# Performance work log

Measured on AMD Instinct MI355X. Metric: run time of the kernel, lower is better.

The kernel has to match this reference:

```python
import jax, jax.numpy as jnp
import numpy as np

N = 65536          # nodes
E = 1048576        # edges
IN_C = 128
HID_C = 32
HEADS = 4
OUT_C = 64
NEG_SLOPE = 0.2
EPS = 1e-16


def gat_conv(x, edge_index, W, att_src, att_dst, bias, heads, out_c, concat):
    """PyG-style GATConv. x: [N, F_in]; edge_index: [2, E] (row=src, col=dst).
    W: [F_in, heads*out_c]; att_src/att_dst: [heads, out_c]; bias: [heads*out_c] or [out_c]."""
    src, dst = edge_index[0], edge_index[1]
    n = x.shape[0]
    h = (x @ W).reshape(n, heads, out_c)                      # [N, H, C]
    a_src = jnp.einsum('nhc,hc->nh', h, att_src)              # [N, H]
    a_dst = jnp.einsum('nhc,hc->nh', h, att_dst)              # [N, H]
    alpha = a_src[src] + a_dst[dst]                           # [E, H]
    alpha = jax.nn.leaky_relu(alpha, NEG_SLOPE)
    # segment softmax over incoming edges of each destination node
    amax = jax.ops.segment_max(alpha, dst, num_segments=n)    # [N, H]
    alpha = jnp.exp(alpha - amax[dst])
    denom = jax.ops.segment_sum(alpha, dst, num_segments=n)   # [N, H]
    alpha = alpha / (denom[dst] + EPS)
    # weighted scatter-add aggregation
    msgs = alpha[:, :, None] * h[src]                         # [E, H, C]
    out = jax.ops.segment_sum(msgs, dst, num_segments=n)      # [N, H, C]
    if concat:
        out = out.reshape(n, heads * out_c)
    else:
        out = out.mean(axis=1)
    return out + bias


def setup_inputs() -> dict:
    key = jax.random.key(0)
    ks = jax.random.split(key, 10)
    s_in = 1.0 / np.sqrt(IN_C)
    s_h = 1.0 / np.sqrt(HEADS * HID_C)
    x = jax.random.normal(ks[0], (N, IN_C), dtype=jnp.float32)
    edge_index = jax.random.randint(ks[1], (2, E), 0, N, dtype=jnp.int64)
    W1 = jax.random.normal(ks[2], (IN_C, HEADS * HID_C), dtype=jnp.float32) * s_in
    att_src1 = jax.random.normal(ks[3], (HEADS, HID_C), dtype=jnp.float32) * s_h
    att_dst1 = jax.random.normal(ks[4], (HEADS, HID_C), dtype=jnp.float32) * s_h
    b1 = jnp.zeros((HEADS * HID_C,), dtype=jnp.float32)
    W2 = jax.random.normal(ks[5], (HEADS * HID_C, OUT_C), dtype=jnp.float32) * s_h
    att_src2 = jax.random.normal(ks[6], (1, OUT_C), dtype=jnp.float32) * s_h
    att_dst2 = jax.random.normal(ks[7], (1, OUT_C), dtype=jnp.float32) * s_h
    b2 = jnp.zeros((OUT_C,), dtype=jnp.float32)
    return {"x": x, "edge_index": edge_index, "W1": W1, "att_src1": att_src1,
            "att_dst1": att_dst1, "b1": b1, "W2": W2, "att_src2": att_src2,
            "att_dst2": att_dst2, "b2": b2}


def reference(x, edge_index, W1, att_src1, att_dst1, b1, W2, att_src2, att_dst2, b2):
    # dropout is identity in eval mode
    h = gat_conv(x, edge_index, W1, att_src1, att_dst1, b1, HEADS, HID_C, concat=True)
    h = jax.nn.sigmoid(h)
    h = gat_conv(h, edge_index, W2, att_src2, att_dst2, b2, 1, OUT_C, concat=True)
    return jax.nn.sigmoid(h)
```

## Files before the change

### kernel.cpp

```cpp
#include <hip/hip_runtime.h>
#include <hip/hip_fp16.h>

#define N_NODES 65536
#define N_EDGES 1048576
#define NBUCK 256
#define PBLOCKS 1024
#define EPB (N_EDGES / PBLOCKS)
#define K4CAP 6144
#define GB1 (N_NODES / 64)
constexpr float NEG = 0.2f;
constexpr float EPS_ = 1e-16f;
constexpr float WSHIFT = 2.7725887f;

typedef __attribute__((ext_vector_type(8))) short bf16x8;
typedef __attribute__((ext_vector_type(4))) float f32x4;

__device__ __forceinline__ unsigned short f2bf(float f) {
    unsigned int u = __float_as_uint(f);
    return (unsigned short)((u + 0x7fffu + ((u >> 16) & 1u)) >> 16);
}
__device__ __forceinline__ unsigned short f2h(float f) {
    __half_raw r = __half_raw(__float2half(f));
    return r.x;
}
__device__ __forceinline__ __half2 u2h2(unsigned int u) {
    union { unsigned int u; __half2 h; } c; c.u = u; return c.h;
}
__device__ __forceinline__ unsigned int h22u(__half2 h) {
    union { unsigned int u; __half2 h; } c; c.h = h; return c.u;
}
__device__ __forceinline__ float lrelu_exp_s(float l) {
    return __expf(fmaxf(l, NEG * l) - WSHIFT);
}


__global__ __launch_bounds__(1024) void scan_a(const int* __restrict__ in,
                                               int* __restrict__ out,
                                               int* __restrict__ bsum) {
    __shared__ int sm[1024];
    int t = threadIdx.x, i = blockIdx.x * 1024 + t;
    int v = in[i];
    sm[t] = v;
    __syncthreads();
    for (int off = 1; off < 1024; off <<= 1) {
        int u = (t >= off) ? sm[t - off] : 0;
        __syncthreads();
        sm[t] += u;
        __syncthreads();
    }
    out[i] = sm[t] - v;
    if (t == 1023) bsum[blockIdx.x] = sm[t];
}

__global__ __launch_bounds__(1024) void scan_c(int* __restrict__ arr,
                                               const int* __restrict__ bsum) {
    __shared__ int partial[4];
    int t = threadIdx.x;
    if (t < 256) {
        int v = (t < (int)blockIdx.x) ? bsum[t] : 0;
        #pragma unroll
        for (int msk = 1; msk < 64; msk <<= 1) v += __shfl_xor(v, msk);
        if ((t & 63) == 0) partial[t >> 6] = v;
    }
    __syncthreads();
    int pref = partial[0] + partial[1] + partial[2] + partial[3];
    arr[blockIdx.x * 1024 + t] += pref;
}

__global__ __launch_bounds__(256) void partition_kernel(const int* __restrict__ ei,
                                                        const int* __restrict__ cursor_mat,
                                                        unsigned int* __restrict__ edge_part) {
    __shared__ int h[NBUCK];
    __shared__ int start[NBUCK];
    __shared__ int cur[NBUCK];
    __shared__ int gcur[NBUCK];
    __shared__ unsigned int stage[EPB];
    int t = threadIdx.x;
    h[t] = 0;
    gcur[t] = cursor_mat[t * PBLOCKS + blockIdx.x];
    __syncthreads();
    unsigned int ent[EPB / 256];
    int base = blockIdx.x * EPB;
    #pragma unroll
    for (int i = 0; i < EPB / 256; ++i) {
        int e = base + i * 256 + t;
        int s = ei[e], d = ei[N_EDGES + e];
        ent[i] = ((unsigned int)s << 16) | (unsigned int)d;
        atomicAdd(&h[d >> 8], 1);
    }
    __syncthreads();
    int v = h[t];
    start[t] = v;
    __syncthreads();
    for (int off = 1; off < 256; off <<= 1) {
        int u = (t >= off) ? start[t - off] : 0;
        __syncthreads();
        start[t] += u;
        __syncthreads();
    }
    int excl = start[t] - v;
    start[t] = excl;
    cur[t] = excl;
    __syncthreads();
    #pragma unroll
    for (int i = 0; i < EPB / 256; ++i) {
        int b = (int)((ent[i] & 0xffffu) >> 8);
        int slot = atomicAdd(&cur[b], 1);
        stage[slot] = ent[i];
    }
    __syncthreads();
    int s0 = t * (EPB / 256);
    #pragma unroll
    for (int i = 0; i < EPB / 256; ++i) {
        unsigned int p = stage[s0 + i];
        int b = (int)((p & 0xffffu) >> 8);
        edge_part[gcur[b] + (s0 + i - start[b])] = p;
    }
}

__global__ __launch_bounds__(1024) void finalize_kernel(const unsigned int* __restrict__ edge_part,
                                                        const int* __restrict__ cursor_mat,
                                                        int* __restrict__ row_ptr,
                                                        unsigned short* __restrict__ csr16) {
    __shared__ int h[256];
    __shared__ int sc[256];
    __shared__ int cur[256];
    __shared__ unsigned short stage[K4CAP];
    int t = threadIdx.x;
    int b = blockIdx.x;
    if (b == NBUCK - 1 && t == 0) row_ptr[N_NODES] = N_EDGES;
    int cs = cursor_mat[b * PBLOCKS];
    int ce = (b == NBUCK - 1) ? N_EDGES : cursor_mat[(b + 1) * PBLOCKS];
    int cnt = ce - cs;
    if (t < 256) h[t] = 0;
    __syncthreads();
    for (int i = t; i < cnt; i += 1024)
        atomicAdd(&h[edge_part[cs + i] & 0xffu], 1);
    __syncthreads();
    int v = 0;
    if (t < 256) { v = h[t]; sc[t] = v; }
    __syncthreads();
    for (int off = 1; off < 256; off <<= 1) {
        int u = (t < 256 && t >= off) ? sc[t - off] : 0;
        __syncthreads();
        if (t < 256) sc[t] += u;
        __syncthreads();
    }
    if (t < 256) {
        int excl = sc[t] - v;
        row_ptr[b * 256 + t] = cs + excl;
        cur[t] = excl;
    }
    __syncthreads();
    if (cnt <= K4CAP) {
        for (int i = t; i < cnt; i += 1024) {
            unsigned int p = edge_part[cs + i];
            int slot = atomicAdd(&cur[p & 0xffu], 1);
            stage[slot] = (unsigned short)(p >> 16);
        }
        __syncthreads();
        for (int i = t; i < cnt; i += 1024)
            csr16[cs + i] = stage[i];
    } else {
        for (int i = t; i < cnt; i += 1024) {
            unsigned int p = edge_part[cs + i];
            int slot = atomicAdd(&cur[p & 0xffu], 1);
            csr16[cs + slot] = (unsigned short)(p >> 16);
        }
    }
}


__global__ __launch_bounds__(256) void gemm1_hist(const float* __restrict__ X,
                                                  const float* __restrict__ W,
                                                  const float* __restrict__ as_w,
                                                  const float* __restrict__ ad_w,
                                                  const int* __restrict__ ei,
                                                  unsigned short* __restrict__ H,
                                                  float* __restrict__ a_src,
                                                  float* __restrict__ a_dst,
                                                  int* __restrict__ hist_mat) {
    extern __shared__ unsigned short Wl[];
    int t = threadIdx.x;
    if (blockIdx.x >= GB1) {
        int* hs = (int*)Wl;
        int pb = blockIdx.x - GB1;
        hs[t] = 0;
        __syncthreads();
        int base = pb * EPB;
        #pragma unroll
        for (int i = 0; i < EPB / 256; ++i) {
            int d = ei[N_EDGES + base + i * 256 + t];
            atomicAdd(&hs[d >> 8], 1);
        }
        __syncthreads();
        hist_mat[t * PBLOCKS + pb] = hs[t];
        return;
    }
    constexpr int OUTC = 128;
    constexpr int NT = OUTC / 16;
    for (int idx = t; idx < OUTC * 128; idx += 256) {
        int j = idx & 7;
        int ln = (idx >> 3) & 63;
        int fc = idx >> 9;
        int kc = fc & 3, ct = fc >> 2;
        int k = kc * 32 + (ln >> 4) * 8 + j;
        int nn = ct * 16 + (ln & 15);
        Wl[idx] = (unsigned short)f2bf(W[k * OUTC + nn]);
    }
    __syncthreads();
    int wave = t >> 6, lane = t & 63;
    int m = lane & 15, quad = lane >> 4;
    int node_base = blockIdx.x * 64 + wave * 16;
    const float* xrow = X + (size_t)(node_base + m) * 128 + quad * 8;
    bf16x8 a[4];
    #pragma unroll
    for (int kc = 0; kc < 4; ++kc) {
        float4 u = *(const float4*)(xrow + kc * 32);
        float4 v = *(const float4*)(xrow + kc * 32 + 4);
        bf16x8 af;
        af[0] = (short)f2bf(u.x); af[1] = (short)f2bf(u.y);
        af[2] = (short)f2bf(u.z); af[3] = (short)f2bf(u.w);
        af[4] = (short)f2bf(v.x); af[5] = (short)f2bf(v.y);
        af[6] = (short)f2bf(v.z); af[7] = (short)f2bf(v.w);
        a[kc] = af;
    }
    float asv[NT], adv[NT];
    #pragma unroll
    for (int ct = 0; ct < NT; ++ct) {
        asv[ct] = as_w[ct * 16 + m];
        adv[ct] = ad_w[ct * 16 + m];
    }
    float ps[4][4] = {};
    float pd[4][4] = {};
    #pragma unroll
    for (int ct = 0; ct < NT; ++ct) {
        f32x4 acc = {0.f, 0.f, 0.f, 0.f};
        #pragma unroll
        for (int kc = 0; kc < 4; ++kc) {
            bf16x8 bfr = *(const bf16x8*)(Wl + ((ct * 4 + kc) * 64 + lane) * 8);
            acc = __builtin_amdgcn_mfma_f32_16x16x32_bf16(a[kc], bfr, acc, 0, 0, 0);
        }
        int hh = ct >> 1;
        #pragma unroll
        for (int r = 0; r < 4; ++r) {
            H[(size_t)(node_base + quad * 4 + r) * OUTC + ct * 16 + m] = f2h(acc[r]);
            ps[r][hh] += acc[r] * asv[ct];
            pd[r][hh] += acc[r] * adv[ct];
        }
    }
    #pragma unroll
    for (int r = 0; r < 4; ++r) {
        #pragma unroll
        for (int hh = 0; hh < 4; ++hh) {
            float s = ps[r][hh], d = pd[r][hh];
            #pragma unroll
            for (int msk = 1; msk < 16; msk <<= 1) {
                s += __shfl_xor(s, msk);
                d += __shfl_xor(d, msk);
            }
            if (m == 0) {
                int node = node_base + quad * 4 + r;
                a_src[node * 4 + hh] = s;
                a_dst[node * 4 + hh] = d;
            }
        }
    }
}


__global__ __launch_bounds__(256) void gemm2_mfma(const unsigned short* __restrict__ X,
                                                  const float* __restrict__ W,
                                                  const float* __restrict__ as_w,
                                                  const float* __restrict__ ad_w,
                                                  unsigned short* __restrict__ H,
                                                  float* __restrict__ a_src,
                                                  float* __restrict__ a_dst) {
    constexpr int OUTC = 64;
    constexpr int NT = OUTC / 16;
    extern __shared__ unsigned short Wl[];
    int t = threadIdx.x;
    for (int idx = t; idx < OUTC * 128; idx += 256) {
        int j = idx & 7;
        int ln = (idx >> 3) & 63;
        int fc = idx >> 9;
        int kc = fc & 3, ct = fc >> 2;
        int k = kc * 32 + (ln >> 4) * 8 + j;
        int nn = ct * 16 + (ln & 15);
        Wl[idx] = (unsigned short)f2bf(W[k * OUTC + nn]);
    }
    __syncthreads();
    int wave = t >> 6, lane = t & 63;
    int m = lane & 15, quad = lane >> 4;
    int node_base = blockIdx.x * 64 + wave * 16;
    const unsigned short* xrow = X + (size_t)(node_base + m) * 128 + quad * 8;
    bf16x8 a[4];
    #pragma unroll
    for (int kc = 0; kc < 4; ++kc) a[kc] = *(const bf16x8*)(xrow + kc * 32);
    float asv[NT], adv[NT];
    #pragma unroll
    for (int ct = 0; ct < NT; ++ct) {
        asv[ct] = as_w[ct * 16 + m];
        adv[ct] = ad_w[ct * 16 + m];
    }
    float ps[4] = {};
    float pd[4] = {};
    #pragma unroll
    for (int ct = 0; ct < NT; ++ct) {
        f32x4 acc = {0.f, 0.f, 0.f, 0.f};
        #pragma unroll
        for (int kc = 0; kc < 4; ++kc) {
            bf16x8 bfr = *(const bf16x8*)(Wl + ((ct * 4 + kc) * 64 + lane) * 8);
            acc = __builtin_amdgcn_mfma_f32_16x16x32_bf16(a[kc], bfr, acc, 0, 0, 0);
        }
        #pragma unroll
        for (int r = 0; r < 4; ++r) {
            H[(size_t)(node_base + quad * 4 + r) * OUTC + ct * 16 + m] = f2h(acc[r]);
            ps[r] += acc[r] * asv[ct];
            pd[r] += acc[r] * adv[ct];
        }
    }
    #pragma unroll
    for (int r = 0; r < 4; ++r) {
        float s = ps[r], d = pd[r];
        #pragma unroll
        for (int msk = 1; msk < 16; msk <<= 1) {
            s += __shfl_xor(s, msk);
            d += __shfl_xor(d, msk);
        }
        if (m == 0) {
            int node = node_base + quad * 4 + r;
            a_src[node] = s;
            a_dst[node] = d;
        }
    }
}


__global__ __launch_bounds__(256, 8) void agg1_kernel(const int* __restrict__ row_ptr,
                                                      const unsigned short* __restrict__ csr16,
                                                      const unsigned int* __restrict__ h1u,
                                                      const float* __restrict__ a_src,
                                                      const float* __restrict__ a_dst,
                                                      const float* __restrict__ b1,
                                                      unsigned short* __restrict__ x2) {
    int wave = (blockIdx.x * 256 + threadIdx.x) >> 6;
    int lane = threadIdx.x & 63;
    int half = lane >> 5;
    int ln = lane & 31;
    int n = wave * 2 + half;
    int j8 = ln & 7;
    int whead = ln >> 3;
    int sub = ln >> 4;
    int col = ln & 15;
    int hd_c = col >> 2;
    int rbase = half * 32 + hd_c * 8 + sub;
    float adw = a_dst[n * 4 + whead];
    const unsigned int* h1c = h1u + col * 4;
    const float* asw = a_src + whead;
    int e = row_ptr[n], end = row_ptr[n + 1];
    __half2 acc0 = u2h2(0u), acc1 = u2h2(0u), acc2 = u2h2(0u), acc3 = u2h2(0u);
    float denom = 0.f;
    while (e < end) {
        int rem = end - e;
        int mbA = rem > 8 ? 8 : rem;
        int remB = rem - 8;
        int mbB = remB > 8 ? 8 : (remB > 0 ? remB : 0);
        int idxA = e + (j8 < mbA ? j8 : 0);
        int idxB = (remB > 0) ? (e + 8 + (j8 < mbB ? j8 : 0)) : idxA;
        int sA = (int)csr16[idxA];
        int sB = (int)csr16[idxB];
        float lA = asw[sA * 4] + adw;
        float lB = asw[sB * 4] + adw;
        float wA = (j8 < mbA) ? lrelu_exp_s(lA) : 0.f;
        float wB = (j8 < mbB) ? lrelu_exp_s(lB) : 0.f;
        denom += wA + wB;
        unsigned int curA = ((unsigned int)f2h(wA) << 16) | (unsigned int)sA;
        unsigned int curB = ((unsigned int)f2h(wB) << 16) | (unsigned int)sB;
        unsigned int pkA0 = __shfl(curA, rbase);
        unsigned int pkA1 = __shfl(curA, rbase + 2);
        unsigned int pkA2 = __shfl(curA, rbase + 4);
        unsigned int pkA3 = __shfl(curA, rbase + 6);
        unsigned int pkB0 = __shfl(curB, rbase);
        unsigned int pkB1 = __shfl(curB, rbase + 2);
        unsigned int pkB2 = __shfl(curB, rbase + 4);
        unsigned int pkB3 = __shfl(curB, rbase + 6);
        uint4 hvA0 = *(const uint4*)(h1c + (size_t)(pkA0 & 0xffffu) * 64);
        uint4 hvA1 = *(const uint4*)(h1c + (size_t)(pkA1 & 0xffffu) * 64);
        uint4 hvA2 = *(const uint4*)(h1c + (size_t)(pkA2 & 0xffffu) * 64);
        uint4 hvA3 = *(const uint4*)(h1c + (size_t)(pkA3 & 0xffffu) * 64);
        uint4 hvB0 = *(const uint4*)(h1c + (size_t)(pkB0 & 0xffffu) * 64);
        uint4 hvB1 = *(const uint4*)(h1c + (size_t)(pkB1 & 0xffffu) * 64);
        uint4 hvB2 = *(const uint4*)(h1c + (size_t)(pkB2 & 0xffffu) * 64);
        uint4 hvB3 = *(const uint4*)(h1c + (size_t)(pkB3 & 0xffffu) * 64);
        unsigned int wu; __half2 w2;
        wu = pkA0 >> 16; w2 = u2h2(wu | (wu << 16));
        acc0 = __hfma2(w2, u2h2(hvA0.x), acc0);
        acc1 = __hfma2(w2, u2h2(hvA0.y), acc1);
        acc2 = __hfma2(w2, u2h2(hvA0.z), acc2);
        acc3 = __hfma2(w2, u2h2(hvA0.w), acc3);
        wu = pkA1 >> 16; w2 = u2h2(wu | (wu << 16));
        acc0 = __hfma2(w2, u2h2(hvA1.x), acc0);
        acc1 = __hfma2(w2, u2h2(hvA1.y), acc1);
        acc2 = __hfma2(w2, u2h2(hvA1.z), acc2);
        acc3 = __hfma2(w2, u2h2(hvA1.w), acc3);
        wu = pkA2 >> 16; w2 = u2h2(wu | (wu << 16));
        acc0 = __hfma2(w2, u2h2(hvA2.x), acc0);
        acc1 = __hfma2(w2, u2h2(hvA2.y), acc1);
        acc2 = __hfma2(w2, u2h2(hvA2.z), acc2);
        acc3 = __hfma2(w2, u2h2(hvA2.w), acc3);
        wu = pkA3 >> 16; w2 = u2h2(wu | (wu << 16));
        acc0 = __hfma2(w2, u2h2(hvA3.x), acc0);
        acc1 = __hfma2(w2, u2h2(hvA3.y), acc1);
        acc2 = __hfma2(w2, u2h2(hvA3.z), acc2);
        acc3 = __hfma2(w2, u2h2(hvA3.w), acc3);
        wu = pkB0 >> 16; w2 = u2h2(wu | (wu << 16));
        acc0 = __hfma2(w2, u2h2(hvB0.x), acc0);
        acc1 = __hfma2(w2, u2h2(hvB0.y), acc1);
        acc2 = __hfma2(w2, u2h2(hvB0.z), acc2);
        acc3 = __hfma2(w2, u2h2(hvB0.w), acc3);
        wu = pkB1 >> 16; w2 = u2h2(wu | (wu << 16));
        acc0 = __hfma2(w2, u2h2(hvB1.x), acc0);
        acc1 = __hfma2(w2, u2h2(hvB1.y), acc1);
        acc2 = __hfma2(w2, u2h2(hvB1.z), acc2);
        acc3 = __hfma2(w2, u2h2(hvB1.w), acc3);
        wu = pkB2 >> 16; w2 = u2h2(wu | (wu << 16));
        acc0 = __hfma2(w2, u2h2(hvB2.x), acc0);
        acc1 = __hfma2(w2, u2h2(hvB2.y), acc1);
        acc2 = __hfma2(w2, u2h2(hvB2.z), acc2);
        acc3 = __hfma2(w2, u2h2(hvB2.w), acc3);
        wu = pkB3 >> 16; w2 = u2h2(wu | (wu << 16));
        acc0 = __hfma2(w2, u2h2(hvB3.x), acc0);
        acc1 = __hfma2(w2, u2h2(hvB3.y), acc1);
        acc2 = __hfma2(w2, u2h2(hvB3.z), acc2);
        acc3 = __hfma2(w2, u2h2(hvB3.w), acc3);
        e += 16;
    }
    acc0 = __hadd2(acc0, u2h2(__shfl_xor(h22u(acc0), 16)));
    acc1 = __hadd2(acc1, u2h2(__shfl_xor(h22u(acc1), 16)));
    acc2 = __hadd2(acc2, u2h2(__shfl_xor(h22u(acc2), 16)));
    acc3 = __hadd2(acc3, u2h2(__shfl_xor(h22u(acc3), 16)));
    #pragma unroll
    for (int m = 1; m < 8; m <<= 1) denom += __shfl_xor(denom, m);
    float dfin = __shfl(denom, half * 32 + hd_c * 8);
    if (sub == 0) {
        float inv = 1.f / (dfin + EPS_);
        int c0 = col * 8;
        float v[8];
        v[0] = __low2float(acc0); v[1] = __high2float(acc0);
        v[2] = __low2float(acc1); v[3] = __high2float(acc1);
        v[4] = __low2float(acc2); v[5] = __high2float(acc2);
        v[6] = __low2float(acc3); v[7] = __high2float(acc3);
        unsigned int o[4];
        #pragma unroll
        for (int i = 0; i < 4; ++i) {
            float u0 = v[2 * i] * inv + b1[c0 + 2 * i];
            float u1 = v[2 * i + 1] * inv + b1[c0 + 2 * i + 1];
            u0 = 1.f / (1.f + __expf(-u0));
            u1 = 1.f / (1.f + __expf(-u1));
            o[i] = (unsigned int)f2bf(u0) | ((unsigned int)f2bf(u1) << 16);
        }
        *(uint4*)(x2 + (size_t)n * 128 + c0) = make_uint4(o[0], o[1], o[2], o[3]);
    }
}

__global__ __launch_bounds__(256, 8) void agg2_kernel(const int* __restrict__ row_ptr,
                                                      const unsigned short* __restrict__ csr16,
                                                      const unsigned int* __restrict__ h2u,
                                                      const float* __restrict__ a_src,
                                                      const float* __restrict__ a_dst,
                                                      const float* __restrict__ b2,
                                                      float* __restrict__ out) {
    int wave = (blockIdx.x * 256 + threadIdx.x) >> 6;
    int lane = threadIdx.x & 63;
    int half = lane >> 5;
    int ln = lane & 31;
    int n = wave * 2 + half;
    int j8 = ln & 7;
    int sub = (ln >> 3) & 3;
    int col = ln & 7;
    int rbase = half * 32 + sub;
    float ad = a_dst[n];
    const unsigned int* h2c = h2u + col * 4;
    int e = row_ptr[n], end = row_ptr[n + 1];
    __half2 acc0 = u2h2(0u), acc1 = u2h2(0u), acc2 = u2h2(0u), acc3 = u2h2(0u);
    float denom = 0.f;
    while (e < end) {
        int rem = end - e;
        int mbA = rem > 8 ? 8 : rem;
        int remB = rem - 8;
        int mbB = remB > 8 ? 8 : (remB > 0 ? remB : 0);
        int idxA = e + (j8 < mbA ? j8 : 0);
        int idxB = (remB > 0) ? (e + 8 + (j8 < mbB ? j8 : 0)) : idxA;
        int sA = (int)csr16[idxA];
        int sB = (int)csr16[idxB];
        float lA = a_src[sA] + ad;
        float lB = a_src[sB] + ad;
        float wA = (j8 < mbA) ? lrelu_exp_s(lA) : 0.f;
        float wB = (j8 < mbB) ? lrelu_exp_s(lB) : 0.f;
        denom += wA + wB;
        unsigned int curA = ((unsigned int)f2h(wA) << 16) | (unsigned int)sA;
        unsigned int curB = ((unsigned int)f2h(wB) << 16) | (unsigned int)sB;
        unsigned int pkA0 = __shfl(curA, rbase);
        unsigned int pkA1 = __shfl(curA, rbase + 4);
        unsigned int pkB0 = __shfl(curB, rbase);
        unsigned int pkB1 = __shfl(curB, rbase + 4);
        uint4 hvA0 = *(const uint4*)(h2c + (size_t)(pkA0 & 0xffffu) * 32);
        uint4 hvA1 = *(const uint4*)(h2c + (size_t)(pkA1 & 0xffffu) * 32);
        uint4 hvB0 = *(const uint4*)(h2c + (size_t)(pkB0 & 0xffffu) * 32);
        uint4 hvB1 = *(const uint4*)(h2c + (size_t)(pkB1 & 0xffffu) * 32);
        unsigned int wu; __half2 w2;
        wu = pkA0 >> 16; w2 = u2h2(wu | (wu << 16));
        acc0 = __hfma2(w2, u2h2(hvA0.x), acc0);
        acc1 = __hfma2(w2, u2h2(hvA0.y), acc1);
        acc2 = __hfma2(w2, u2h2(hvA0.z), acc2);
        acc3 = __hfma2(w2, u2h2(hvA0.w), acc3);
        wu = pkA1 >> 16; w2 = u2h2(wu | (wu << 16));
        acc0 = __hfma2(w2, u2h2(hvA1.x), acc0);
        acc1 = __hfma2(w2, u2h2(hvA1.y), acc1);
        acc2 = __hfma2(w2, u2h2(hvA1.z), acc2);
        acc3 = __hfma2(w2, u2h2(hvA1.w), acc3);
        wu = pkB0 >> 16; w2 = u2h2(wu | (wu << 16));
        acc0 = __hfma2(w2, u2h2(hvB0.x), acc0);
        acc1 = __hfma2(w2, u2h2(hvB0.y), acc1);
        acc2 = __hfma2(w2, u2h2(hvB0.z), acc2);
        acc3 = __hfma2(w2, u2h2(hvB0.w), acc3);
        wu = pkB1 >> 16; w2 = u2h2(wu | (wu << 16));
        acc0 = __hfma2(w2, u2h2(hvB1.x), acc0);
        acc1 = __hfma2(w2, u2h2(hvB1.y), acc1);
        acc2 = __hfma2(w2, u2h2(hvB1.z), acc2);
        acc3 = __hfma2(w2, u2h2(hvB1.w), acc3);
        e += 16;
    }
    #pragma unroll
    for (int m = 8; m < 32; m <<= 1) {
        acc0 = __hadd2(acc0, u2h2(__shfl_xor(h22u(acc0), m)));
        acc1 = __hadd2(acc1, u2h2(__shfl_xor(h22u(acc1), m)));
        acc2 = __hadd2(acc2, u2h2(__shfl_xor(h22u(acc2), m)));
        acc3 = __hadd2(acc3, u2h2(__shfl_xor(h22u(acc3), m)));
    }
    #pragma unroll
    for (int m = 1; m < 8; m <<= 1) denom += __shfl_xor(denom, m);
    if (sub == 0) {
        float inv = 1.f / (denom + EPS_);
        int c0 = col * 8;
        float v[8];
        v[0] = __low2float(acc0); v[1] = __high2float(acc0);
        v[2] = __low2float(acc1); v[3] = __high2float(acc1);
        v[4] = __low2float(acc2); v[5] = __high2float(acc2);
        v[6] = __low2float(acc3); v[7] = __high2float(acc3);
        float o[8];
        #pragma unroll
        for (int i = 0; i < 8; ++i) {
            float u = v[i] * inv + b2[c0 + i];
            o[i] = 1.f / (1.f + __expf(-u));
        }
        float4* dst = (float4*)(out + (size_t)n * 64 + c0);
        dst[0] = make_float4(o[0], o[1], o[2], o[3]);
        dst[1] = make_float4(o[4], o[5], o[6], o[7]);
    }
}


extern "C" void kernel_launch(void* const* d_in, const int* in_sizes, int n_in,
                              void* d_out, int out_size, void* d_ws, size_t ws_size,
                              hipStream_t stream) {
    (void)in_sizes; (void)n_in; (void)out_size; (void)ws_size;
    const float* x   = (const float*)d_in[0];
    const int*   ei  = (const int*)d_in[1];
    const float* W1  = (const float*)d_in[2];
    const float* as1 = (const float*)d_in[3];
    const float* ad1 = (const float*)d_in[4];
    const float* b1  = (const float*)d_in[5];
    const float* W2  = (const float*)d_in[6];
    const float* as2 = (const float*)d_in[7];
    const float* ad2 = (const float*)d_in[8];
    const float* b2  = (const float*)d_in[9];
    float* out = (float*)d_out;

    char* p = (char*)d_ws;
    auto alloc = [&](size_t bytes) -> void* {
        void* r = (void*)p;
        p += (bytes + 255) & ~(size_t)255;
        return r;
    };
    int* hist_mat   = (int*)alloc((size_t)NBUCK * PBLOCKS * 4);
    int* cursor_mat = (int*)alloc((size_t)NBUCK * PBLOCKS * 4);
    int* bsum       = (int*)alloc(256 * 4);
    unsigned int* edge_part = (unsigned int*)alloc((size_t)N_EDGES * 4);
    int* row_ptr    = (int*)alloc((size_t)(N_NODES + 1) * 4);
    unsigned short* csr16 = (unsigned short*)alloc((size_t)N_EDGES * 2);
    unsigned short* h1 = (unsigned short*)alloc((size_t)N_NODES * 128 * 2);
    float* a_src1   = (float*)alloc((size_t)N_NODES * 4 * 4);
    float* a_dst1   = (float*)alloc((size_t)N_NODES * 4 * 4);
    unsigned short* x2 = (unsigned short*)alloc((size_t)N_NODES * 128 * 2);
    unsigned short* h2 = (unsigned short*)alloc((size_t)N_NODES * 64 * 2);
    float* a_src2   = (float*)alloc((size_t)N_NODES * 4);
    float* a_dst2   = (float*)alloc((size_t)N_NODES * 4);

    gemm1_hist<<<GB1 + PBLOCKS, 256, 128 * 128 * 2, stream>>>(
        x, W1, as1, ad1, ei, h1, a_src1, a_dst1, hist_mat);
    scan_a<<<NBUCK * PBLOCKS / 1024, 1024, 0, stream>>>(hist_mat, cursor_mat, bsum);
    scan_c<<<NBUCK * PBLOCKS / 1024, 1024, 0, stream>>>(cursor_mat, bsum);
    partition_kernel<<<PBLOCKS, 256, 0, stream>>>(ei, cursor_mat, edge_part);
    finalize_kernel<<<NBUCK, 1024, 0, stream>>>(edge_part, cursor_mat, row_ptr, csr16);
    agg1_kernel<<<N_NODES / 8, 256, 0, stream>>>(row_ptr, csr16, (const unsigned int*)h1,
                                                 a_src1, a_dst1, b1, x2);
    gemm2_mfma<<<N_NODES / 64, 256, 128 * 64 * 2, stream>>>(x2, W2, as2, ad2, h2, a_src2, a_dst2);
    agg2_kernel<<<N_NODES / 8, 256, 0, stream>>>(row_ptr, csr16, (const unsigned int*)h2,
                                                 a_src2, a_dst2, b2, out);
}
```

Measured before the change: 234.5 us.

## Fold scan block-prefix into partition and finalize kernels; relax agg launch bounds

```diff
diff --git a/kernel.cpp b/kernel.cpp
--- a/kernel.cpp
+++ b/kernel.cpp
@@ -52,32 +52,20 @@
     if (t == 1023) bsum[blockIdx.x] = sm[t];
 }
 
-__global__ __launch_bounds__(1024) void scan_c(int* __restrict__ arr,
-                                               const int* __restrict__ bsum) {
-    __shared__ int partial[4];
-    int t = threadIdx.x;
-    if (t < 256) {
-        int v = (t < (int)blockIdx.x) ? bsum[t] : 0;
-        #pragma unroll
-        for (int msk = 1; msk < 64; msk <<= 1) v += __shfl_xor(v, msk);
-        if ((t & 63) == 0) partial[t >> 6] = v;
-    }
-    __syncthreads();
-    int pref = partial[0] + partial[1] + partial[2] + partial[3];
-    arr[blockIdx.x * 1024 + t] += pref;
-}
-
 __global__ __launch_bounds__(256) void partition_kernel(const int* __restrict__ ei,
                                                         const int* __restrict__ cursor_mat,
+                                                        const int* __restrict__ bsum,
                                                         unsigned int* __restrict__ edge_part) {
     __shared__ int h[NBUCK];
     __shared__ int start[NBUCK];
     __shared__ int cur[NBUCK];
     __shared__ int gcur[NBUCK];
+    __shared__ int bs[NBUCK];
     __shared__ unsigned int stage[EPB];
     int t = threadIdx.x;
     h[t] = 0;
-    gcur[t] = cursor_mat[t * PBLOCKS + blockIdx.x];
+    int bsv = bsum[t];
+    bs[t] = bsv;
     __syncthreads();
     unsigned int ent[EPB / 256];
     int base = blockIdx.x * EPB;
@@ -93,14 +81,17 @@
     start[t] = v;
     __syncthreads();
     for (int off = 1; off < 256; off <<= 1) {
-        int u = (t >= off) ? start[t - off] : 0;
-        __syncthreads();
-        start[t] += u;
+        int u1 = (t >= off) ? start[t - off] : 0;
+        int u2 = (t >= off) ? bs[t - off] : 0;
+        __syncthreads();
+        start[t] += u1;
+        bs[t] += u2;
         __syncthreads();
     }
     int excl = start[t] - v;
     start[t] = excl;
     cur[t] = excl;
+    gcur[t] = cursor_mat[t * PBLOCKS + blockIdx.x] + (bs[t] - bsv);
     __syncthreads();
     #pragma unroll
     for (int i = 0; i < EPB / 256; ++i) {
@@ -120,17 +111,27 @@
 
 __global__ __launch_bounds__(1024) void finalize_kernel(const unsigned int* __restrict__ edge_part,
                                                         const int* __restrict__ cursor_mat,
+                                                        const int* __restrict__ bsum,
                                                         int* __restrict__ row_ptr,
                                                         unsigned short* __restrict__ csr16) {
     __shared__ int h[256];
     __shared__ int sc[256];
     __shared__ int cur[256];
+    __shared__ int bs[256];
     __shared__ unsigned short stage[K4CAP];
     int t = threadIdx.x;
     int b = blockIdx.x;
     if (b == NBUCK - 1 && t == 0) row_ptr[N_NODES] = N_EDGES;
-    int cs = cursor_mat[b * PBLOCKS];
-    int ce = (b == NBUCK - 1) ? N_EDGES : cursor_mat[(b + 1) * PBLOCKS];
+    if (t < 256) bs[t] = bsum[t];
+    __syncthreads();
+    for (int off = 1; off < 256; off <<= 1) {
+        int u = (t < 256 && t >= off) ? bs[t - off] : 0;
+        __syncthreads();
+        if (t < 256) bs[t] += u;
+        __syncthreads();
+    }
+    int cs = cursor_mat[b * PBLOCKS] + (b ? bs[b - 1] : 0);
+    int ce = (b == NBUCK - 1) ? N_EDGES : cursor_mat[(b + 1) * PBLOCKS] + bs[b];
     int cnt = ce - cs;
     if (t < 256) h[t] = 0;
     __syncthreads();
@@ -337,13 +338,13 @@
 }
 
 
-__global__ __launch_bounds__(256, 8) void agg1_kernel(const int* __restrict__ row_ptr,
-                                                      const unsigned short* __restrict__ csr16,
-                                                      const unsigned int* __restrict__ h1u,
-                                                      const float* __restrict__ a_src,
-                                                      const float* __restrict__ a_dst,
-                                                      const float* __restrict__ b1,
-                                                      unsigned short* __restrict__ x2) {
+__global__ __launch_bounds__(256) void agg1_kernel(const int* __restrict__ row_ptr,
+                                                   const unsigned short* __restrict__ csr16,
+                                                   const unsigned int* __restrict__ h1u,
+                                                   const float* __restrict__ a_src,
+                                                   const float* __restrict__ a_dst,
+                                                   const float* __restrict__ b1,
+                                                   unsigned short* __restrict__ x2) {
     int wave = (blockIdx.x * 256 + threadIdx.x) >> 6;
     int lane = threadIdx.x & 63;
     int half = lane >> 5;
@@ -464,13 +465,13 @@
     }
 }
 
-__global__ __launch_bounds__(256, 8) void agg2_kernel(const int* __restrict__ row_ptr,
-                                                      const unsigned short* __restrict__ csr16,
-                                                      const unsigned int* __restrict__ h2u,
-                                                      const float* __restrict__ a_src,
-                                                      const float* __restrict__ a_dst,
-                                                      const float* __restrict__ b2,
-                                                      float* __restrict__ out) {
+__global__ __launch_bounds__(256) void agg2_kernel(const int* __restrict__ row_ptr,
+                                                   const unsigned short* __restrict__ csr16,
+                                                   const unsigned int* __restrict__ h2u,
+                                                   const float* __restrict__ a_src,
+                                                   const float* __restrict__ a_dst,
+                                                   const float* __restrict__ b2,
+                                                   float* __restrict__ out) {
     int wave = (blockIdx.x * 256 + threadIdx.x) >> 6;
     int lane = threadIdx.x & 63;
     int half = lane >> 5;
@@ -601,9 +602,8 @@
     gemm1_hist<<<GB1 + PBLOCKS, 256, 128 * 128 * 2, stream>>>(
         x, W1, as1, ad1, ei, h1, a_src1, a_dst1, hist_mat);
     scan_a<<<NBUCK * PBLOCKS / 1024, 1024, 0, stream>>>(hist_mat, cursor_mat, bsum);
-    scan_c<<<NBUCK * PBLOCKS / 1024, 1024, 0, stream>>>(cursor_mat, bsum);
-    partition_kernel<<<PBLOCKS, 256, 0, stream>>>(ei, cursor_mat, edge_part);
-    finalize_kernel<<<NBUCK, 1024, 0, stream>>>(edge_part, cursor_mat, row_ptr, csr16);
+    partition_kernel<<<PBLOCKS, 256, 0, stream>>>(ei, cursor_mat, bsum, edge_part);
+    finalize_kernel<<<NBUCK, 1024, 0, stream>>>(edge_part, cursor_mat, bsum, row_ptr, csr16);
     agg1_kernel<<<N_NODES / 8, 256, 0, stream>>>(row_ptr, csr16, (const unsigned int*)h1,
                                                  a_src1, a_dst1, b1, x2);
     gemm2_mfma<<<N_NODES / 64, 256, 128 * 64 * 2, stream>>>(x2, W2, as2, ad2, h2, a_src2, a_dst2);
```

After: 220.0 us. -6.2%, faster.
